# Kernel optimization log

Hardware: AMD Instinct MI355X
Metric: run time of the kernel (lower is better)

## Reference

```python
import jax, jax.numpy as jnp
import numpy as np

H = 256  # GRU hidden size


def _gru_scan(state, lengths, Wih, Whh, bih, bhh):
    # state: [B, T, D]; run a batched GRU over time, freezing h once t >= lengths[b]
    B, T, D = state.shape
    # precompute input gates for all timesteps: [T, B, 3H]
    gi_all = jnp.einsum('btd,gd->tbg', state, Wih) + bih

    def step(h, inp):
        gi, t = inp
        gh = h @ Whh.T + bhh                       # [B, 3H]
        i_r, i_z, i_n = jnp.split(gi, 3, axis=-1)
        h_r, h_z, h_n = jnp.split(gh, 3, axis=-1)
        r = jax.nn.sigmoid(i_r + h_r)
        z = jax.nn.sigmoid(i_z + h_z)
        n = jnp.tanh(i_n + r * h_n)
        h_new = (1.0 - z) * n + z * h              # torch GRUCell update
        mask = (t < lengths)[:, None]              # ragged: stop updating past length
        return jnp.where(mask, h_new, h), None

    h0 = jnp.zeros((B, H), state.dtype)
    h, _ = jax.lax.scan(step, h0, (gi_all, jnp.arange(T)))
    return h  # [B, H] = hidden after lengths[b] GRU steps


def _mlp(x, w1, b1, w2, b2, w3, b3, w4, b4, wq, bq):
    x = jax.nn.relu(x @ w1.T + b1)
    x = jax.nn.relu(x @ w2.T + b2)
    x = jax.nn.relu(x @ w3.T + b3)
    x = jax.nn.relu(x @ w4.T + b4)
    return x @ wq.T + bq  # [B, 1]


def setup_inputs() -> dict:
    key = jax.random.key(0)
    ks = jax.random.split(key, 40)
    B, T, D, A = 2048, 64, 15, 1
    inp = {}
    inp['state'] = jax.random.normal(ks[0], (B, T, D), jnp.float32)
    inp['action'] = jax.random.normal(ks[1], (B, A), jnp.float32)
    inp['lengths'] = jax.random.randint(ks[2], (B,), 1, T + 1, jnp.int32)
    i = 3
    for t in (1, 2):
        for name, shape, fan in [('Wih', (3 * H, D), D), ('Whh', (3 * H, H), H),
                                 ('bih', (3 * H,), H), ('bhh', (3 * H,), H)]:
            inp[f'g{t}_{name}'] = jax.random.normal(ks[i], shape, jnp.float32) / np.sqrt(fan)
            i += 1
        for name, (o, n) in [('fc1', (1024, H + D + A)), ('fc2', (1024, 1024)),
                             ('fc3', (512, 1024)), ('fc4', (256, 512)), ('q', (1, 256))]:
            inp[f'{name}_{t}_w'] = jax.random.normal(ks[i], (o, n), jnp.float32) / np.sqrt(n)
            i += 1
            inp[f'{name}_{t}_b'] = jax.random.normal(ks[i], (o,), jnp.float32) * 0.01
            i += 1
    return inp


def reference(state, action, lengths,
              g1_Wih, g1_Whh, g1_bih, g1_bhh,
              fc1_1_w, fc1_1_b, fc2_1_w, fc2_1_b, fc3_1_w, fc3_1_b,
              fc4_1_w, fc4_1_b, q_1_w, q_1_b,
              g2_Wih, g2_Whh, g2_bih, g2_bhh,
              fc1_2_w, fc1_2_b, fc2_2_w, fc2_2_b, fc3_2_w, fc3_2_b,
              fc4_2_w, fc4_2_b, q_2_w, q_2_b):
    h1 = _gru_scan(state, lengths, g1_Wih, g1_Whh, g1_bih, g1_bhh)
    h2 = _gru_scan(state, lengths, g2_Wih, g2_Whh, g2_bih, g2_bhh)
    aug = jnp.concatenate([state[:, 0, :], action], axis=-1)  # [B, 16]
    x1 = jnp.concatenate([aug, h1], axis=-1)                  # [B, 272]
    x2 = jnp.concatenate([aug, h2], axis=-1)
    out1 = _mlp(x1, fc1_1_w, fc1_1_b, fc2_1_w, fc2_1_b, fc3_1_w, fc3_1_b,
                fc4_1_w, fc4_1_b, q_1_w, q_1_b)
    out2 = _mlp(x2, fc1_2_w, fc1_2_b, fc2_2_w, fc2_2_b, fc3_2_w, fc3_2_b,
                fc4_2_w, fc4_2_b, q_2_w, q_2_b)
    return (out1, out2)
```

## Files before the change

### kernel.cpp

```cpp
#include <hip/hip_runtime.h>

typedef float  f32x4 __attribute__((ext_vector_type(4)));
typedef short  s16x8 __attribute__((ext_vector_type(8)));
typedef __bf16 b16x8 __attribute__((ext_vector_type(8)));

#define DEV __device__ __forceinline__

DEV unsigned short f2b(float f) {
  unsigned u = __builtin_bit_cast(unsigned, f);
  u = (u + 0x7FFFu + ((u >> 16) & 1u)) >> 16;
  return (unsigned short)u;
}
DEV b16x8 ld8(const unsigned short* p) {
  return __builtin_bit_cast(b16x8, *(const s16x8*)p);
}
DEV float sigm(float x) { return __builtin_amdgcn_rcpf(1.f + __expf(-x)); }
DEV float tanh_fast(float x) {
  float e = __expf(2.f * x);
  return 1.f - 2.f * __builtin_amdgcn_rcpf(e + 1.f);
}
DEV void async16(const unsigned short* g, unsigned short* l) {
  __builtin_amdgcn_global_load_lds(
      (const __attribute__((address_space(1))) unsigned int*)g,
      (__attribute__((address_space(3))) unsigned int*)l, 16, 0, 0);
}
DEV f32x4 mfma_bf16(b16x8 a, b16x8 b, f32x4 c) {
  return __builtin_amdgcn_mfma_f32_16x16x32_bf16(a, b, c, 0, 0, 0);
}

struct PrepArgs {
  const float *whh[2], *wih[2], *bih[2], *bhh[2];
  const float *src[2][4];
  unsigned short *waug[2], *dst[2][4];
  const float *qb[2];
  float *out;
};

__global__ __launch_bounds__(256) void prep_kernel(PrepArgs p) {
  const int job = blockIdx.y;
  const int i0 = blockIdx.x * 256 + threadIdx.x;
  const int stride = gridDim.x * 256;
  if (job < 2) {
    const float* whh = p.whh[job];
    const float* wih = p.wih[job];
    const float* bih = p.bih[job];
    const float* bhh = p.bhh[job];
    unsigned short* dst = p.waug[job];
    for (int idx = i0; idx < 768 * 288; idx += stride) {
      int j = idx / 288, k = idx - j * 288;
      float v = 0.f;
      if (k < 256) {
        int o = k & 31;
        int kk = (k & 0x1E0) + (o >> 1) + ((o & 1) << 4);
        v = whh[j * 256 + kk];
      } else if (k < 271)  v = wih[j * 15 + (k - 256)];
      else if (k == 271)   v = (j < 512) ? (bih[j] + bhh[j]) : bih[j];
      dst[idx] = f2b(v);
    }
  } else if (job < 10) {
    const int jj = job - 2, br = jj >> 2, ly = jj & 3;
    const int rowsA[4] = {1024, 1024, 512, 256};
    const int scA[4]   = {272, 1024, 1024, 512};
    const int dcA[4]   = {288, 1024, 1024, 512};
    const float* src = p.src[br][ly];
    unsigned short* dst = p.dst[br][ly];
    const int sc = scA[ly], dc = dcA[ly], tot = rowsA[ly] * dc;
    for (int idx = i0; idx < tot; idx += stride) {
      int r = idx / dc, c = idx - r * dc;
      float v = (c < sc) ? src[r * sc + c] : 0.f;
      dst[idx] = f2b(v);
    }
  } else {
    for (int idx = i0; idx < 4096; idx += stride)
      p.out[idx] = p.qb[idx >> 11][0];
  }
}

#define GRU_LDS_BYTES 147584
__attribute__((amdgpu_waves_per_eu(1, 1)))
__global__ void __launch_bounds__(256) gru_kernel(
    const float* __restrict__ state, const float* __restrict__ action,
    const int* __restrict__ lengths,
    const unsigned short* __restrict__ waug0, const unsigned short* __restrict__ waug1,
    const float* __restrict__ bhh0, const float* __restrict__ bhh1,
    unsigned short* __restrict__ x0, unsigned short* __restrict__ x1) {
  extern __shared__ char smem[];
  unsigned short* W7   = (unsigned short*)smem;
  unsigned short* WA   = (unsigned short*)(smem + 49152);
  unsigned short* SgL  = (unsigned short*)(smem + 98304);
  unsigned*       Hb2  = (unsigned*)(smem + 131072);
  int* lenS = (int*)(smem + 147456);
  int* mlS  = (int*)(smem + 147520);

  const int tid = threadIdx.x;
  const int lane = tid & 63, w = tid >> 6;
  const int l15 = lane & 15, q = lane >> 4;
  const int g = blockIdx.x & 1;
  const int r0 = (blockIdx.x >> 1) * 16;

  const unsigned short* Waug = g ? waug1 : waug0;
  const float* bhh = g ? bhh1 : bhh0;
  unsigned short* xout = g ? x1 : x0;

  for (int i = tid; i < 4096; i += 256) Hb2[i] = 0;
  if (tid < 16) lenS[tid] = lengths[r0 + tid];
  for (int s = tid; s < 64 * 32; s += 256) {
    const int t = s >> 5, L = s & 31;
    const int q2 = L >> 4, r = L & 15;
    const float* sp = state + (size_t)(r0 + r) * 960 + t * 15;
    s16x8 h;
#pragma unroll
    for (int j = 0; j < 8; j++) {
      const int k = q2 * 8 + j;
      float v = (k < 15) ? sp[k] : (k == 15 ? 1.0f : 0.f);
      h[j] = (short)f2b(v);
    }
    *(s16x8*)(SgL + (size_t)s * 8) = h;
  }
  __syncthreads();
  if (tid == 0) {
    int m = 1;
    for (int i = 0; i < 16; i++) m = lenS[i] > m ? lenS[i] : m;
    *mlS = m;
  }

  int c0[12];
#pragma unroll
  for (int gate = 0; gate < 3; gate++)
#pragma unroll
    for (int j = 0; j < 4; j++) c0[gate * 4 + j] = gate * 256 + 64 * w + 16 * j;

  b16x8 wres[12][7];
#pragma unroll
  for (int i = 0; i < 12; i++) {
    const unsigned short* bpi = Waug + (size_t)(c0[i] + l15) * 288 + q * 8;
#pragma unroll
    for (int j = 0; j < 7; j++) wres[i][j] = ld8(bpi + j * 32);
    *(s16x8*)(W7 + ((size_t)i * 256 + tid) * 8) =
        __builtin_bit_cast(s16x8, ld8(bpi + 7 * 32));
    *(s16x8*)(WA + ((size_t)i * 256 + tid) * 8) =
        __builtin_bit_cast(s16x8, ld8(bpi + 256));
  }
  float bnH[4];
#pragma unroll
  for (int j = 0; j < 4; j++) bnH[j] = bhh[c0[8 + j] + l15];
  int len4[4];
#pragma unroll
  for (int r = 0; r < 4; r++) len4[r] = lenS[q * 4 + r];

  int aOff[8];
#pragma unroll
  for (int k = 0; k < 8; k++) {
    const int ck = 4 * k + q;
    const int pk = (ck & 24) | ((ck & 7) ^ (l15 & 7));
    aOff[k] = l15 * 128 + pk * 4;
  }
  int wOff[2][4];
#pragma unroll
  for (int p = 0; p < 2; p++)
#pragma unroll
    for (int rg = 0; rg < 4; rg++) {
      const int row = q * 4 + rg;
      const int cb = 8 * w + 4 * p + (l15 >> 2);
      const int pw = (cb & 24) | ((cb & 7) ^ (row & 7));
      wOff[p][rg] = row * 128 + pw * 4 + (l15 & 3);
    }
  __syncthreads();
  const int maxlen = *mlS;

  float hold[4][4] = {{0,0,0,0},{0,0,0,0},{0,0,0,0},{0,0,0,0}};
  int poff = 0;

  for (int t = 0; t < maxlen; ++t) {
    __syncthreads();

    f32x4 acc[12];
#pragma unroll
    for (int i = 0; i < 12; i++) acc[i] = f32x4{0.f, 0.f, 0.f, 0.f};

    {
      b16x8 a8 = ld8(SgL + t * 256 + ((q & 1) * 16 + l15) * 8);
#pragma unroll
      for (int i = 0; i < 12; i++) {
        b16x8 bw = ld8(WA + ((size_t)i * 256 + tid) * 8);
        acc[i] = mfma_bf16(a8, bw, acc[i]);
      }
    }
    f32x4 giN[4];
#pragma unroll
    for (int j = 0; j < 4; j++) { giN[j] = acc[8 + j]; acc[8 + j] = acc[8 + j] + bnH[j]; }

    const unsigned* hb = Hb2 + poff;
#pragma unroll
    for (int k = 0; k < 7; k++) {
      b16x8 a = __builtin_bit_cast(b16x8, *(const uint4*)(hb + aOff[k]));
#pragma unroll
      for (int i = 0; i < 12; i++) acc[i] = mfma_bf16(a, wres[i][k], acc[i]);
    }
    {
      b16x8 a = __builtin_bit_cast(b16x8, *(const uint4*)(hb + aOff[7]));
#pragma unroll
      for (int i = 0; i < 12; i++) {
        b16x8 bw = ld8(W7 + ((size_t)i * 256 + tid) * 8);
        acc[i] = mfma_bf16(a, bw, acc[i]);
      }
    }

    unsigned* hbw = Hb2 + (poff ^ 2048);
#pragma unroll
    for (int j = 0; j < 4; j++)
#pragma unroll
      for (int rg = 0; rg < 4; rg++) {
        const bool live = (t < len4[rg]);
        float r = sigm(acc[j][rg]);
        float z = sigm(acc[4 + j][rg]);
        float n = tanh_fast(giN[j][rg] + r * (acc[8 + j][rg] - giN[j][rg]));
        float h = n + z * (hold[j][rg] - n);
        h = live ? h : hold[j][rg];
        hold[j][rg] = h;
      }
#pragma unroll
    for (int p = 0; p < 2; p++)
#pragma unroll
      for (int rg = 0; rg < 4; rg++)
        hbw[wOff[p][rg]] = (unsigned)f2b(hold[2 * p][rg]) |
                           ((unsigned)f2b(hold[2 * p + 1][rg]) << 16);
    poff ^= 2048;
  }

#pragma unroll
  for (int j = 0; j < 4; j++)
#pragma unroll
    for (int rg = 0; rg < 4; rg++) {
      const int row = q * 4 + rg;
      xout[(size_t)(r0 + row) * 288 + 16 + c0[j] + l15] = f2b(hold[j][rg]);
    }
  for (int s = tid; s < 512; s += 256) {
    const int row = s >> 5, cc = s & 31;
    float v; int col;
    if (cc < 15)       { v = state[(size_t)(r0 + row) * 960 + cc]; col = cc; }
    else if (cc == 15) { v = action[r0 + row]; col = 15; }
    else               { v = 0.f; col = 256 + cc; }
    xout[(size_t)(r0 + row) * 288 + col] = f2b(v);
  }
}

template <int BM, int BN>
__global__ __launch_bounds__(256, 4) void gemm_bias_relu(
    const unsigned short* __restrict__ A0, const unsigned short* __restrict__ A1,
    const unsigned short* __restrict__ W0, const unsigned short* __restrict__ W1,
    const float* __restrict__ b0, const float* __restrict__ b1,
    unsigned short* __restrict__ Y0, unsigned short* __restrict__ Y1,
    int N, int K) {
  const unsigned short* A = blockIdx.z ? A1 : A0;
  const unsigned short* W = blockIdx.z ? W1 : W0;
  const float* bias = blockIdx.z ? b1 : b0;
  unsigned short* Y = blockIdx.z ? Y1 : Y0;

  constexpr int MT = BM / 32;
  constexpr int NT = BN / 32;
  const int tid = threadIdx.x;
  const int lane = tid & 63, wid = tid >> 6;
  const int wm = wid >> 1, wn = wid & 1;
  const int l15 = lane & 15, q = lane >> 4;
  const int m0 = blockIdx.x * BM, n0 = blockIdx.y * BN;

  __shared__ unsigned short As[BM * 32];
  __shared__ unsigned short Bs[BN * 32];

  f32x4 acc[MT][NT];
#pragma unroll
  for (int mi = 0; mi < MT; mi++)
#pragma unroll
    for (int ni = 0; ni < NT; ni++) acc[mi][ni] = f32x4{0.f, 0.f, 0.f, 0.f};

  const int srow = tid >> 2, scol = (tid & 3) * 8;

  for (int k0 = 0; k0 < K; k0 += 32) {
#pragma unroll
    for (int g64 = 0; g64 < BM / 64; g64++)
      async16(A + (size_t)(m0 + g64 * 64 + srow) * K + scol + k0,
              &As[g64 * 2048 + tid * 8]);
#pragma unroll
    for (int g64 = 0; g64 < BN / 64; g64++)
      async16(W + (size_t)(n0 + g64 * 64 + srow) * K + scol + k0,
              &Bs[g64 * 2048 + tid * 8]);
    __syncthreads();

    b16x8 af[MT], bf[NT];
#pragma unroll
    for (int mi = 0; mi < MT; mi++)
      af[mi] = ld8(&As[(wm * (BM / 2) + mi * 16 + l15) * 32 + q * 8]);
#pragma unroll
    for (int ni = 0; ni < NT; ni++)
      bf[ni] = ld8(&Bs[(wn * (BN / 2) + ni * 16 + l15) * 32 + q * 8]);
#pragma unroll
    for (int mi = 0; mi < MT; mi++)
#pragma unroll
      for (int ni = 0; ni < NT; ni++)
        acc[mi][ni] = mfma_bf16(af[mi], bf[ni], acc[mi][ni]);
    __syncthreads();
  }

#pragma unroll
  for (int ni = 0; ni < NT; ni++) {
    const int col = n0 + wn * (BN / 2) + ni * 16 + l15;
    const float bv = bias[col];
#pragma unroll
    for (int mi = 0; mi < MT; mi++) {
      const int rbase = m0 + wm * (BM / 2) + mi * 16 + q * 4;
#pragma unroll
      for (int rg = 0; rg < 4; rg++) {
        float v = acc[mi][ni][rg] + bv;
        v = fmaxf(v, 0.f);
        Y[(size_t)(rbase + rg) * N + col] = f2b(v);
      }
    }
  }
}

__global__ __launch_bounds__(256, 4) void fc4q_kernel(
    const unsigned short* __restrict__ A0, const unsigned short* __restrict__ A1,
    const unsigned short* __restrict__ W0, const unsigned short* __restrict__ W1,
    const float* __restrict__ b0, const float* __restrict__ b1,
    const float* __restrict__ qw0, const float* __restrict__ qw1,
    float* __restrict__ out) {
  const unsigned short* A = blockIdx.z ? A1 : A0;
  const unsigned short* W = blockIdx.z ? W1 : W0;
  const float* bias = blockIdx.z ? b1 : b0;
  const float* qw = blockIdx.z ? qw1 : qw0;

  const int tid = threadIdx.x;
  const int lane = tid & 63, wn = tid >> 6;
  const int l15 = lane & 15, q = lane >> 4;
  const int m0 = blockIdx.x * 32;
  const int nbase = blockIdx.y * 128;
  const int K = 512;

  __shared__ unsigned short As[32 * 32];
  __shared__ unsigned short Bs[128 * 32];
  __shared__ float red[32][4];

  f32x4 acc[2][2];
#pragma unroll
  for (int mi = 0; mi < 2; mi++)
#pragma unroll
    for (int ni = 0; ni < 2; ni++) acc[mi][ni] = f32x4{0.f, 0.f, 0.f, 0.f};

  const int srow = tid >> 2, scol = (tid & 3) * 8;
  for (int k0 = 0; k0 < K; k0 += 32) {
    if (tid < 128)
      async16(A + (size_t)(m0 + srow) * K + scol + k0, &As[tid * 8]);
#pragma unroll
    for (int g64 = 0; g64 < 2; g64++)
      async16(W + (size_t)(nbase + g64 * 64 + srow) * K + scol + k0,
              &Bs[g64 * 2048 + tid * 8]);
    __syncthreads();

    b16x8 af[2], bf[2];
#pragma unroll
    for (int mi = 0; mi < 2; mi++)
      af[mi] = ld8(&As[(mi * 16 + l15) * 32 + q * 8]);
#pragma unroll
    for (int ni = 0; ni < 2; ni++)
      bf[ni] = ld8(&Bs[(wn * 32 + ni * 16 + l15) * 32 + q * 8]);
#pragma unroll
    for (int mi = 0; mi < 2; mi++)
#pragma unroll
      for (int ni = 0; ni < 2; ni++)
        acc[mi][ni] = mfma_bf16(af[mi], bf[ni], acc[mi][ni]);
    __syncthreads();
  }

#pragma unroll
  for (int mi = 0; mi < 2; mi++) {
#pragma unroll
    for (int rg = 0; rg < 4; rg++) {
      float s = 0.f;
#pragma unroll
      for (int ni = 0; ni < 2; ni++) {
        const int col = nbase + wn * 32 + ni * 16 + l15;
        float v = fmaxf(acc[mi][ni][rg] + bias[col], 0.f);
        s += v * qw[col];
      }
#pragma unroll
      for (int off = 1; off < 16; off <<= 1) s += __shfl_xor(s, off);
      if (l15 == 0) red[mi * 16 + q * 4 + rg][wn] = s;
    }
  }
  __syncthreads();
  if (tid < 32) {
    float t = red[tid][0] + red[tid][1] + red[tid][2] + red[tid][3];
    atomicAdd(out + (size_t)blockIdx.z * 2048 + m0 + tid, t);
  }
}

extern "C" void kernel_launch(void* const* d_in, const int* in_sizes, int n_in,
                              void* d_out, int out_size, void* d_ws, size_t ws_size,
                              hipStream_t stream) {
  const float* state   = (const float*)d_in[0];
  const float* action  = (const float*)d_in[1];
  const int*   lengths = (const int*)d_in[2];
  const float* g_wih[2] = {(const float*)d_in[3], (const float*)d_in[17]};
  const float* g_whh[2] = {(const float*)d_in[4], (const float*)d_in[18]};
  const float* g_bih[2] = {(const float*)d_in[5], (const float*)d_in[19]};
  const float* g_bhh[2] = {(const float*)d_in[6], (const float*)d_in[20]};
  const float* fcw[2][4] = {
      {(const float*)d_in[7], (const float*)d_in[9], (const float*)d_in[11], (const float*)d_in[13]},
      {(const float*)d_in[21], (const float*)d_in[23], (const float*)d_in[25], (const float*)d_in[27]}};
  const float* fcb[2][4] = {
      {(const float*)d_in[8], (const float*)d_in[10], (const float*)d_in[12], (const float*)d_in[14]},
      {(const float*)d_in[22], (const float*)d_in[24], (const float*)d_in[26], (const float*)d_in[28]}};
  const float* qw[2] = {(const float*)d_in[15], (const float*)d_in[29]};
  const float* qb[2] = {(const float*)d_in[16], (const float*)d_in[30]};
  float* out = (float*)d_out;

  uintptr_t base = (uintptr_t)d_ws;
  auto alloc = [&](size_t bytes) -> unsigned short* {
    void* p = (void*)base;
    base += (bytes + 255) & ~(size_t)255;
    return (unsigned short*)p;
  };
  unsigned short *waug[2], *w1b[2], *w2b[2], *w3b[2], *w4b[2], *xb[2], *yA[2], *yB[2];
  for (int g = 0; g < 2; g++) waug[g] = alloc(768 * 288 * 2);
  for (int g = 0; g < 2; g++) w1b[g] = alloc(1024 * 288 * 2);
  for (int g = 0; g < 2; g++) w2b[g] = alloc(1024 * 1024 * 2);
  for (int g = 0; g < 2; g++) w3b[g] = alloc(512 * 1024 * 2);
  for (int g = 0; g < 2; g++) w4b[g] = alloc(256 * 512 * 2);
  for (int g = 0; g < 2; g++) xb[g] = alloc(2048 * 288 * 2);
  for (int g = 0; g < 2; g++) yA[g] = alloc(2048 * 1024 * 2);
  for (int g = 0; g < 2; g++) yB[g] = alloc(2048 * 1024 * 2);
  (void)ws_size; (void)in_sizes; (void)n_in; (void)out_size;

  PrepArgs pa;
  for (int g = 0; g < 2; g++) {
    pa.whh[g] = g_whh[g]; pa.wih[g] = g_wih[g];
    pa.bih[g] = g_bih[g]; pa.bhh[g] = g_bhh[g];
    pa.waug[g] = waug[g];
    pa.src[g][0] = fcw[g][0]; pa.dst[g][0] = w1b[g];
    pa.src[g][1] = fcw[g][1]; pa.dst[g][1] = w2b[g];
    pa.src[g][2] = fcw[g][2]; pa.dst[g][2] = w3b[g];
    pa.src[g][3] = fcw[g][3]; pa.dst[g][3] = w4b[g];
    pa.qb[g] = qb[g];
  }
  pa.out = out;
  prep_kernel<<<dim3(64, 11), 256, 0, stream>>>(pa);

  (void)hipFuncSetAttribute((const void*)gru_kernel,
                            hipFuncAttributeMaxDynamicSharedMemorySize,
                            GRU_LDS_BYTES);
  gru_kernel<<<dim3(256), dim3(256), GRU_LDS_BYTES, stream>>>(
      state, action, lengths, waug[0], waug[1], g_bhh[0], g_bhh[1], xb[0], xb[1]);

  gemm_bias_relu<64, 64><<<dim3(32, 16, 2), 256, 0, stream>>>(
      xb[0], xb[1], w1b[0], w1b[1], fcb[0][0], fcb[1][0], yA[0], yA[1], 1024, 288);
  gemm_bias_relu<64, 64><<<dim3(32, 16, 2), 256, 0, stream>>>(
      yA[0], yA[1], w2b[0], w2b[1], fcb[0][1], fcb[1][1], yB[0], yB[1], 1024, 1024);
  gemm_bias_relu<64, 64><<<dim3(32, 8, 2), 256, 0, stream>>>(
      yB[0], yB[1], w3b[0], w3b[1], fcb[0][2], fcb[1][2], yA[0], yA[1], 512, 1024);
  fc4q_kernel<<<dim3(64, 2, 2), 256, 0, stream>>>(
      yA[0], yA[1], w4b[0], w4b[1], fcb[0][3], fcb[1][3], qw[0], qw[1], out);
}
```

Before: 356.2 us.

## Double-buffer MLP GEMMs with register prefetch and reorder GRU input MFMAs

```diff
diff --git a/kernel.cpp b/kernel.cpp
--- a/kernel.cpp
+++ b/kernel.cpp
@@ -18,11 +18,6 @@
 DEV float tanh_fast(float x) {
   float e = __expf(2.f * x);
   return 1.f - 2.f * __builtin_amdgcn_rcpf(e + 1.f);
-}
-DEV void async16(const unsigned short* g, unsigned short* l) {
-  __builtin_amdgcn_global_load_lds(
-      (const __attribute__((address_space(1))) unsigned int*)g,
-      (__attribute__((address_space(3))) unsigned int*)l, 16, 0, 0);
 }
 DEV f32x4 mfma_bf16(b16x8 a, b16x8 b, f32x4 c) {
   return __builtin_amdgcn_mfma_f32_16x16x32_bf16(a, b, c, 0, 0, 0);
@@ -61,7 +56,7 @@
     const int jj = job - 2, br = jj >> 2, ly = jj & 3;
     const int rowsA[4] = {1024, 1024, 512, 256};
     const int scA[4]   = {272, 1024, 1024, 512};
-    const int dcA[4]   = {288, 1024, 1024, 512};
+    const int dcA[4]   = {320, 1024, 1024, 512};
     const float* src = p.src[br][ly];
     unsigned short* dst = p.dst[br][ly];
     const int sc = scA[ly], dc = dcA[ly], tot = rowsA[ly] * dc;
@@ -178,19 +173,9 @@
 #pragma unroll
     for (int i = 0; i < 12; i++) acc[i] = f32x4{0.f, 0.f, 0.f, 0.f};
 
-    {
-      b16x8 a8 = ld8(SgL + t * 256 + ((q & 1) * 16 + l15) * 8);
-#pragma unroll
-      for (int i = 0; i < 12; i++) {
-        b16x8 bw = ld8(WA + ((size_t)i * 256 + tid) * 8);
-        acc[i] = mfma_bf16(a8, bw, acc[i]);
-      }
-    }
-    f32x4 giN[4];
-#pragma unroll
-    for (int j = 0; j < 4; j++) { giN[j] = acc[8 + j]; acc[8 + j] = acc[8 + j] + bnH[j]; }
-
     const unsigned* hb = Hb2 + poff;
+    b16x8 a8 = ld8(SgL + t * 256 + ((q & 1) * 16 + l15) * 8);
+
 #pragma unroll
     for (int k = 0; k < 7; k++) {
       b16x8 a = __builtin_bit_cast(b16x8, *(const uint4*)(hb + aOff[k]));
@@ -205,6 +190,17 @@
         acc[i] = mfma_bf16(a, bw, acc[i]);
       }
     }
+    f32x4 accNa[4];
+#pragma unroll
+    for (int i = 0; i < 8; i++) {
+      b16x8 bw = ld8(WA + ((size_t)i * 256 + tid) * 8);
+      acc[i] = mfma_bf16(a8, bw, acc[i]);
+    }
+#pragma unroll
+    for (int j = 0; j < 4; j++) {
+      b16x8 bw = ld8(WA + ((size_t)(8 + j) * 256 + tid) * 8);
+      accNa[j] = mfma_bf16(a8, bw, f32x4{0.f, 0.f, 0.f, 0.f});
+    }
 
     unsigned* hbw = Hb2 + (poff ^ 2048);
 #pragma unroll
@@ -212,9 +208,11 @@
 #pragma unroll
       for (int rg = 0; rg < 4; rg++) {
         const bool live = (t < len4[rg]);
+        float inn = accNa[j][rg];
+        float hn = acc[8 + j][rg] + bnH[j];
         float r = sigm(acc[j][rg]);
         float z = sigm(acc[4 + j][rg]);
-        float n = tanh_fast(giN[j][rg] + r * (acc[8 + j][rg] - giN[j][rg]));
+        float n = tanh_fast(inn + r * hn);
         float h = n + z * (hold[j][rg] - n);
         h = live ? h : hold[j][rg];
         hold[j][rg] = h;
@@ -233,20 +231,21 @@
 #pragma unroll
     for (int rg = 0; rg < 4; rg++) {
       const int row = q * 4 + rg;
-      xout[(size_t)(r0 + row) * 288 + 16 + c0[j] + l15] = f2b(hold[j][rg]);
-    }
-  for (int s = tid; s < 512; s += 256) {
-    const int row = s >> 5, cc = s & 31;
+      xout[(size_t)(r0 + row) * 320 + 16 + c0[j] + l15] = f2b(hold[j][rg]);
+    }
+  for (int s = tid; s < 1024; s += 256) {
+    const int row = s >> 6, cc = s & 63;
     float v; int col;
     if (cc < 15)       { v = state[(size_t)(r0 + row) * 960 + cc]; col = cc; }
     else if (cc == 15) { v = action[r0 + row]; col = 15; }
     else               { v = 0.f; col = 256 + cc; }
-    xout[(size_t)(r0 + row) * 288 + col] = f2b(v);
-  }
-}
-
-template <int BM, int BN>
-__global__ __launch_bounds__(256, 4) void gemm_bias_relu(
+    xout[(size_t)(r0 + row) * 320 + col] = f2b(v);
+  }
+}
+
+DEV int slotOf(int c) { return (c & ~7) | ((c & 7) ^ ((c >> 3) & 7)); }
+
+__global__ __launch_bounds__(256, 4) void gemm_dbuf(
     const unsigned short* __restrict__ A0, const unsigned short* __restrict__ A1,
     const unsigned short* __restrict__ W0, const unsigned short* __restrict__ W1,
     const float* __restrict__ b0, const float* __restrict__ b1,
@@ -257,58 +256,80 @@
   const float* bias = blockIdx.z ? b1 : b0;
   unsigned short* Y = blockIdx.z ? Y1 : Y0;
 
-  constexpr int MT = BM / 32;
-  constexpr int NT = BN / 32;
   const int tid = threadIdx.x;
   const int lane = tid & 63, wid = tid >> 6;
   const int wm = wid >> 1, wn = wid & 1;
   const int l15 = lane & 15, q = lane >> 4;
-  const int m0 = blockIdx.x * BM, n0 = blockIdx.y * BN;
-
-  __shared__ unsigned short As[BM * 32];
-  __shared__ unsigned short Bs[BN * 32];
-
-  f32x4 acc[MT][NT];
-#pragma unroll
-  for (int mi = 0; mi < MT; mi++)
-#pragma unroll
-    for (int ni = 0; ni < NT; ni++) acc[mi][ni] = f32x4{0.f, 0.f, 0.f, 0.f};
-
-  const int srow = tid >> 2, scol = (tid & 3) * 8;
-
-  for (int k0 = 0; k0 < K; k0 += 32) {
-#pragma unroll
-    for (int g64 = 0; g64 < BM / 64; g64++)
-      async16(A + (size_t)(m0 + g64 * 64 + srow) * K + scol + k0,
-              &As[g64 * 2048 + tid * 8]);
-#pragma unroll
-    for (int g64 = 0; g64 < BN / 64; g64++)
-      async16(W + (size_t)(n0 + g64 * 64 + srow) * K + scol + k0,
-              &Bs[g64 * 2048 + tid * 8]);
+  const int m0 = blockIdx.x * 64, n0 = blockIdx.y * 64;
+
+  __shared__ unsigned short As[2][4096];
+  __shared__ unsigned short Bs[2][4096];
+
+  f32x4 acc[2][2];
+#pragma unroll
+  for (int mi = 0; mi < 2; mi++)
+#pragma unroll
+    for (int ni = 0; ni < 2; ni++) acc[mi][ni] = f32x4{0.f, 0.f, 0.f, 0.f};
+
+  const int c0c = tid * 2, c1c = tid * 2 + 1;
+  const int ar0 = c0c >> 3, ak0 = (c0c & 7) * 8;
+  const int ar1 = c1c >> 3, ak1 = (c1c & 7) * 8;
+  const int ws0 = slotOf(c0c) * 8, ws1 = slotOf(c1c) * 8;
+  const unsigned short* pa0 = A + (size_t)(m0 + ar0) * K + ak0;
+  const unsigned short* pa1 = A + (size_t)(m0 + ar1) * K + ak1;
+  const unsigned short* pb0 = W + (size_t)(n0 + ar0) * K + ak0;
+  const unsigned short* pb1 = W + (size_t)(n0 + ar1) * K + ak1;
+
+  const int niter = K >> 6;
+  s16x8 ra0 = *(const s16x8*)pa0, ra1 = *(const s16x8*)pa1;
+  s16x8 rb0 = *(const s16x8*)pb0, rb1 = *(const s16x8*)pb1;
+  *(s16x8*)&As[0][ws0] = ra0; *(s16x8*)&As[0][ws1] = ra1;
+  *(s16x8*)&Bs[0][ws0] = rb0; *(s16x8*)&Bs[0][ws1] = rb1;
+
+  for (int it = 0; it < niter; ++it) {
+    const unsigned short* as = As[it & 1];
+    const unsigned short* bs = Bs[it & 1];
+    const bool pf = (it + 1 < niter);
+    if (pf) {
+      const int k0 = (it + 1) << 6;
+      ra0 = *(const s16x8*)(pa0 + k0); ra1 = *(const s16x8*)(pa1 + k0);
+      rb0 = *(const s16x8*)(pb0 + k0); rb1 = *(const s16x8*)(pb1 + k0);
+    }
     __syncthreads();
 
-    b16x8 af[MT], bf[NT];
-#pragma unroll
-    for (int mi = 0; mi < MT; mi++)
-      af[mi] = ld8(&As[(wm * (BM / 2) + mi * 16 + l15) * 32 + q * 8]);
-#pragma unroll
-    for (int ni = 0; ni < NT; ni++)
-      bf[ni] = ld8(&Bs[(wn * (BN / 2) + ni * 16 + l15) * 32 + q * 8]);
-#pragma unroll
-    for (int mi = 0; mi < MT; mi++)
-#pragma unroll
-      for (int ni = 0; ni < NT; ni++)
-        acc[mi][ni] = mfma_bf16(af[mi], bf[ni], acc[mi][ni]);
-    __syncthreads();
-  }
-
-#pragma unroll
-  for (int ni = 0; ni < NT; ni++) {
-    const int col = n0 + wn * (BN / 2) + ni * 16 + l15;
+#pragma unroll
+    for (int s = 0; s < 2; s++) {
+      b16x8 af[2], bf[2];
+#pragma unroll
+      for (int mi = 0; mi < 2; mi++) {
+        const int ml = wm * 32 + mi * 16 + l15;
+        af[mi] = ld8(as + slotOf(ml * 8 + s * 4 + q) * 8);
+      }
+#pragma unroll
+      for (int ni = 0; ni < 2; ni++) {
+        const int nl = wn * 32 + ni * 16 + l15;
+        bf[ni] = ld8(bs + slotOf(nl * 8 + s * 4 + q) * 8);
+      }
+#pragma unroll
+      for (int mi = 0; mi < 2; mi++)
+#pragma unroll
+        for (int ni = 0; ni < 2; ni++)
+          acc[mi][ni] = mfma_bf16(af[mi], bf[ni], acc[mi][ni]);
+    }
+    if (pf) {
+      const int nb = (it + 1) & 1;
+      *(s16x8*)&As[nb][ws0] = ra0; *(s16x8*)&As[nb][ws1] = ra1;
+      *(s16x8*)&Bs[nb][ws0] = rb0; *(s16x8*)&Bs[nb][ws1] = rb1;
+    }
+  }
+
+#pragma unroll
+  for (int ni = 0; ni < 2; ni++) {
+    const int col = n0 + wn * 32 + ni * 16 + l15;
     const float bv = bias[col];
 #pragma unroll
-    for (int mi = 0; mi < MT; mi++) {
-      const int rbase = m0 + wm * (BM / 2) + mi * 16 + q * 4;
+    for (int mi = 0; mi < 2; mi++) {
+      const int rbase = m0 + wm * 32 + mi * 16 + q * 4;
 #pragma unroll
       for (int rg = 0; rg < 4; rg++) {
         float v = acc[mi][ni][rg] + bv;
@@ -317,6 +338,12 @@
       }
     }
   }
+}
+
+DEV void async16(const unsigned short* g, unsigned short* l) {
+  __builtin_amdgcn_global_load_lds(
+      (const __attribute__((address_space(1))) unsigned int*)g,
+      (__attribute__((address_space(3))) unsigned int*)l, 16, 0, 0);
 }
 
 __global__ __launch_bounds__(256, 4) void fc4q_kernel(
@@ -423,11 +450,11 @@
   };
   unsigned short *waug[2], *w1b[2], *w2b[2], *w3b[2], *w4b[2], *xb[2], *yA[2], *yB[2];
   for (int g = 0; g < 2; g++) waug[g] = alloc(768 * 288 * 2);
-  for (int g = 0; g < 2; g++) w1b[g] = alloc(1024 * 288 * 2);
+  for (int g = 0; g < 2; g++) w1b[g] = alloc(1024 * 320 * 2);
   for (int g = 0; g < 2; g++) w2b[g] = alloc(1024 * 1024 * 2);
   for (int g = 0; g < 2; g++) w3b[g] = alloc(512 * 1024 * 2);
   for (int g = 0; g < 2; g++) w4b[g] = alloc(256 * 512 * 2);
-  for (int g = 0; g < 2; g++) xb[g] = alloc(2048 * 288 * 2);
+  for (int g = 0; g < 2; g++) xb[g] = alloc(2048 * 320 * 2);
   for (int g = 0; g < 2; g++) yA[g] = alloc(2048 * 1024 * 2);
   for (int g = 0; g < 2; g++) yB[g] = alloc(2048 * 1024 * 2);
   (void)ws_size; (void)in_sizes; (void)n_in; (void)out_size;
@@ -452,11 +479,11 @@
   gru_kernel<<<dim3(256), dim3(256), GRU_LDS_BYTES, stream>>>(
       state, action, lengths, waug[0], waug[1], g_bhh[0], g_bhh[1], xb[0], xb[1]);
 
-  gemm_bias_relu<64, 64><<<dim3(32, 16, 2), 256, 0, stream>>>(
-      xb[0], xb[1], w1b[0], w1b[1], fcb[0][0], fcb[1][0], yA[0], yA[1], 1024, 288);
-  gemm_bias_relu<64, 64><<<dim3(32, 16, 2), 256, 0, stream>>>(
+  gemm_dbuf<<<dim3(32, 16, 2), 256, 0, stream>>>(
+      xb[0], xb[1], w1b[0], w1b[1], fcb[0][0], fcb[1][0], yA[0], yA[1], 1024, 320);
+  gemm_dbuf<<<dim3(32, 16, 2), 256, 0, stream>>>(
       yA[0], yA[1], w2b[0], w2b[1], fcb[0][1], fcb[1][1], yB[0], yB[1], 1024, 1024);
-  gemm_bias_relu<64, 64><<<dim3(32, 8, 2), 256, 0, stream>>>(
+  gemm_dbuf<<<dim3(32, 8, 2), 256, 0, stream>>>(
       yB[0], yB[1], w3b[0], w3b[1], fcb[0][2], fcb[1][2], yA[0], yA[1], 512, 1024);
   fc4q_kernel<<<dim3(64, 2, 2), 256, 0, stream>>>(
       yA[0], yA[1], w4b[0], w4b[1], fcb[0][3], fcb[1][3], qw[0], qw[1], out);
```

New measurement: 360.8 us. No clear change (+1.3%).
